# Performance work log

Measured on AMD Instinct MI355X. Metric: run time of the kernel, lower is better.

Reference implementation:

```python
import jax, jax.numpy as jnp
import numpy as np

DIM = 1024
DIM_INNER = 2048
B, S = 4, 4096


def setup_inputs() -> dict:
    key = jax.random.key(0)
    k1, k2, k3 = jax.random.split(key, 3)
    x = jax.random.normal(k1, (B, S, DIM), dtype=jnp.float32)
    # torch Linear weight init ~ U(-1/sqrt(fan_in), 1/sqrt(fan_in)); scaled normals are fine
    W_hg = jax.random.normal(k2, (DIM, 2 * DIM_INNER), dtype=jnp.float32) / np.sqrt(DIM)
    W_out = jax.random.normal(k3, (DIM_INNER, DIM), dtype=jnp.float32) / np.sqrt(DIM_INNER)
    return {"x": x, "W_hg": W_hg, "W_out": W_out}


def heinsen_associative_scan_log(log_coeffs, log_values):
    # a_star[t] = sum_{i<=t} log_coeffs[i]
    a_star = jnp.cumsum(log_coeffs, axis=1)
    log_h0_plus_b_star = jax.lax.cumlogsumexp(log_values - a_star, axis=1)
    return jnp.exp(a_star + log_h0_plus_b_star)


def reference(x, W_hg, W_out):
    # fused projection then split into hidden / gate, each [B, S, DIM_INNER]
    hg = jnp.einsum('bsd,de->bse', x, W_hg)
    hidden, gate = jnp.split(hg, 2, axis=-1)
    # seq_len > 1, prev_hidden = None path of the torch module
    log_z = jax.nn.log_sigmoid(gate)                 # log sigmoid(gate)
    log_coeffs = -jax.nn.softplus(gate)              # log(1 - sigmoid(gate))
    hidden_log = jnp.log(jax.nn.relu(hidden) + 0.5)  # log(g(hidden)) as coded (relu+0.5)
    log_values = hidden_log + log_z
    h = heinsen_associative_scan_log(log_coeffs, log_values)  # [B, S, DIM_INNER]
    out = jnp.einsum('bse,ed->bsd', h, W_out)
    return out
```

## Files before the change

kernel.cpp:

```cpp
#include <hip/hip_runtime.h>
#include <stdint.h>

#define DIMX 1024
#define DIM_INNER 2048
#define BATCH 4
#define SEQ 4096
#define M_TOTAL (BATCH * SEQ)
#define N_HG (2 * DIM_INNER)
#define NCHUNK 32
#define CLEN 128

typedef unsigned short u16;
typedef __attribute__((ext_vector_type(8))) short short8;
typedef __attribute__((ext_vector_type(4))) float floatx4;

__device__ __forceinline__ float bflo(uint32_t u) { return __uint_as_float(u << 16); }
__device__ __forceinline__ float bfhi(uint32_t u) { return __uint_as_float(u & 0xffff0000u); }
__device__ __forceinline__ uint32_t f2bf_bits(float f) {
    uint32_t u = __float_as_uint(f);
    return (u + 0x7fffu + ((u >> 16) & 1u)) >> 16;
}

__global__ __launch_bounds__(256) void prep(const float* __restrict__ x,
                                            const float* __restrict__ Whg,
                                            const float* __restrict__ Wout,
                                            u16* __restrict__ xb,
                                            u16* __restrict__ whgt,
                                            u16* __restrict__ woutt) {
    __shared__ float tile[64][65];
    const int bid = blockIdx.x;
    const int tid = threadIdx.x;
    if (bid < 2048) {
        const int n4 = M_TOTAL * DIMX / 4;
        const float4* in4 = (const float4*)x;
        ushort4* out4 = (ushort4*)xb;
        for (int i = bid * 256 + tid; i < n4; i += 2048 * 256) {
            float4 v = in4[i];
            ushort4 o;
            o.x = (u16)f2bf_bits(v.x);
            o.y = (u16)f2bf_bits(v.y);
            o.z = (u16)f2bf_bits(v.z);
            o.w = (u16)f2bf_bits(v.w);
            out4[i] = o;
        }
        return;
    }
    const float* in;
    u16* out;
    int R, C, tb;
    if (bid < 3072) {
        in = Whg; out = whgt; R = DIMX; C = N_HG; tb = bid - 2048;
    } else {
        in = Wout; out = woutt; R = DIM_INNER; C = DIMX; tb = bid - 3072;
    }
    const int tilesx = C / 64;
    const int c0 = (tb % tilesx) * 64, r0 = (tb / tilesx) * 64;
    const int tx = tid & 63, ty = tid >> 6;
#pragma unroll
    for (int i = ty; i < 64; i += 4)
        tile[i][tx] = in[(size_t)(r0 + i) * C + c0 + tx];
    __syncthreads();
#pragma unroll
    for (int i = ty; i < 64; i += 4)
        out[(size_t)(c0 + i) * R + r0 + tx] = (u16)f2bf_bits(tile[tx][i]);
}

__global__ __launch_bounds__(256, 2) void gemm1_k(const u16* __restrict__ A,
                                                  const u16* __restrict__ Bt,
                                                  uint32_t* __restrict__ av,
                                                  float2* __restrict__ sumAV) {
    __shared__ alignas(16) char smem[65536];
    u16* As = (u16*)smem;
    u16* Bh = (u16*)(smem + 8192);
    u16* Bg = (u16*)(smem + 16384);
    uint32_t* avl = (uint32_t*)smem;

    const int tid = threadIdx.x;
    const int lane = tid & 63;
    const int wave = tid >> 6;
    const int wm = (wave >> 1) * 64;
    const int wn = (wave & 1) * 64;
    const size_t m0 = (size_t)blockIdx.y * 128;
    const int n0 = blockIdx.x * 128;

    floatx4 acch[4][4], accg[4][4];
#pragma unroll
    for (int i = 0; i < 4; ++i)
#pragma unroll
        for (int j = 0; j < 4; ++j) {
            acch[i][j] = (floatx4){0.f, 0.f, 0.f, 0.f};
            accg[i][j] = (floatx4){0.f, 0.f, 0.f, 0.f};
        }

    const int srow = lane >> 2;
    const int scol = ((lane & 3) ^ ((srow >> 1) & 3)) * 8;
    const u16* Ag = A + m0 * DIMX + (size_t)(wave * 16 + srow) * DIMX + scol;
    const u16* Bhg = Bt + (size_t)n0 * DIMX + (size_t)(wave * 16 + srow) * DIMX + scol;
    const u16* Bgg = Bt + (size_t)(DIM_INNER + n0) * DIMX + (size_t)(wave * 16 + srow) * DIMX + scol;
    u16* Asw = As + (wave * 16) * 32;
    u16* Bhw = Bh + (wave * 16) * 32;
    u16* Bgw = Bg + (wave * 16) * 32;

    const int fr = lane & 15;
    const int kblk = lane >> 4;
    const int koff = (kblk ^ ((fr >> 1) & 3)) * 8;

    for (int k0 = 0; k0 < DIMX; k0 += 32) {
        __syncthreads();
#pragma unroll
        for (int i = 0; i < 2; ++i) {
            __builtin_amdgcn_global_load_lds(
                (const __attribute__((address_space(1))) uint32_t*)(const void*)(Ag + (size_t)i * 64 * DIMX + k0),
                (__attribute__((address_space(3))) uint32_t*)(void*)(Asw + i * 64 * 32), 16, 0, 0);
            __builtin_amdgcn_global_load_lds(
                (const __attribute__((address_space(1))) uint32_t*)(const void*)(Bhg + (size_t)i * 64 * DIMX + k0),
                (__attribute__((address_space(3))) uint32_t*)(void*)(Bhw + i * 64 * 32), 16, 0, 0);
            __builtin_amdgcn_global_load_lds(
                (const __attribute__((address_space(1))) uint32_t*)(const void*)(Bgg + (size_t)i * 64 * DIMX + k0),
                (__attribute__((address_space(3))) uint32_t*)(void*)(Bgw + i * 64 * 32), 16, 0, 0);
        }
        __syncthreads();

        short8 af[4], bhf[4], bgf[4];
#pragma unroll
        for (int i = 0; i < 4; ++i)
            af[i] = *(const short8*)(As + (wm + i * 16 + fr) * 32 + koff);
#pragma unroll
        for (int j = 0; j < 4; ++j) {
            bhf[j] = *(const short8*)(Bh + (wn + j * 16 + fr) * 32 + koff);
            bgf[j] = *(const short8*)(Bg + (wn + j * 16 + fr) * 32 + koff);
        }
#pragma unroll
        for (int i = 0; i < 4; ++i)
#pragma unroll
            for (int j = 0; j < 4; ++j) {
                acch[i][j] = __builtin_amdgcn_mfma_f32_16x16x32_bf16(af[i], bhf[j], acch[i][j], 0, 0, 0);
                accg[i][j] = __builtin_amdgcn_mfma_f32_16x16x32_bf16(af[i], bgf[j], accg[i][j], 0, 0, 0);
            }
    }
    __syncthreads();

    const int r0row = (lane >> 4) * 4;
#pragma unroll
    for (int i = 0; i < 4; ++i) {
#pragma unroll
        for (int r = 0; r < 4; ++r) {
            const int row = wm + i * 16 + r0row + r;
#pragma unroll
            for (int j = 0; j < 4; ++j) {
                const int col = wn + j * 16 + fr;
                float h = acch[i][j][r];
                float g = accg[i][j][r];
                g = fminf(fmaxf(g, -30.f), 30.f);
                float e = __expf(-g);
                float z = 1.f / (1.f + e);
                float a = e * z;
                float v = z * (fmaxf(h, 0.f) + 0.5f);
                uint32_t pk = f2bf_bits(a) | (f2bf_bits(v) << 16);
                avl[row * 128 + col] = pk;
                av[(m0 + row) * 2048 + n0 + col] = pk;
            }
        }
    }
    __syncthreads();

    const int col = tid & 127;
    const int rlo = (tid >> 7) * 64;
    float Aa = 1.f, Vv = 0.f;
#pragma unroll 8
    for (int j = 0; j < 64; ++j) {
        uint32_t pk = avl[(rlo + j) * 128 + col];
        float a = bflo(pk), v = bfhi(pk);
        Vv = fmaf(a, Vv, v);
        Aa *= a;
    }
    __syncthreads();
    if (tid < 128) {
        avl[col] = __float_as_uint(Aa);
        avl[128 + col] = __float_as_uint(Vv);
    }
    __syncthreads();
    if (tid >= 128) {
        float Al = __uint_as_float(avl[col]);
        float Vl = __uint_as_float(avl[128 + col]);
        float At = Al * Aa;
        float Vt = fmaf(Aa, Vl, Vv);
        const int chunk = (int)(m0 >> 7);
        sumAV[(size_t)chunk * 2048 + n0 + col] = (float2){At, Vt};
    }
}

__global__ __launch_bounds__(256, 2) void gemm2_k(const u16* __restrict__ A,
                                                  const u16* __restrict__ Bt,
                                                  float* __restrict__ C) {
    const int N = DIMX, K = DIM_INNER;
    __shared__ alignas(16) u16 As[256 * 32];
    __shared__ alignas(16) u16 Bs[128 * 32];

    const int tid = threadIdx.x;
    const int lane = tid & 63;
    const int wave = tid >> 6;
    const int wm = wave * 64;
    const size_t m0 = (size_t)blockIdx.y * 256;
    const size_t n0 = (size_t)blockIdx.x * 128;

    floatx4 acc[4][8];
#pragma unroll
    for (int i = 0; i < 4; ++i)
#pragma unroll
        for (int j = 0; j < 8; ++j) acc[i][j] = (floatx4){0.f, 0.f, 0.f, 0.f};

    const int srow = lane >> 2;
    const int scol = ((lane & 3) ^ ((srow >> 1) & 3)) * 8;
    const u16* Ag = A + (m0 + wave * 16 + srow) * K + scol;
    const u16* Bg = Bt + (n0 + wave * 16 + srow) * K + scol;
    u16* Asw = As + (wave * 16) * 32;
    u16* Bsw = Bs + (wave * 16) * 32;

    const int fr = lane & 15;
    const int kblk = lane >> 4;
    const int koff = (kblk ^ ((fr >> 1) & 3)) * 8;

    for (int k0 = 0; k0 < K; k0 += 32) {
        __syncthreads();
#pragma unroll
        for (int i = 0; i < 4; ++i)
            __builtin_amdgcn_global_load_lds(
                (const __attribute__((address_space(1))) uint32_t*)(const void*)(Ag + (size_t)i * 64 * K + k0),
                (__attribute__((address_space(3))) uint32_t*)(void*)(Asw + i * 64 * 32), 16, 0, 0);
#pragma unroll
        for (int i = 0; i < 2; ++i)
            __builtin_amdgcn_global_load_lds(
                (const __attribute__((address_space(1))) uint32_t*)(const void*)(Bg + (size_t)i * 64 * K + k0),
                (__attribute__((address_space(3))) uint32_t*)(void*)(Bsw + i * 64 * 32), 16, 0, 0);
        __syncthreads();

        short8 af[4], bf[8];
#pragma unroll
        for (int i = 0; i < 4; ++i)
            af[i] = *(const short8*)(As + (wm + i * 16 + fr) * 32 + koff);
#pragma unroll
        for (int j = 0; j < 8; ++j)
            bf[j] = *(const short8*)(Bs + (j * 16 + fr) * 32 + koff);
#pragma unroll
        for (int i = 0; i < 4; ++i)
#pragma unroll
            for (int j = 0; j < 8; ++j)
                acc[i][j] = __builtin_amdgcn_mfma_f32_16x16x32_bf16(af[i], bf[j], acc[i][j], 0, 0, 0);
    }

    const int r0row = (lane >> 4) * 4;
#pragma unroll
    for (int i = 0; i < 4; ++i)
#pragma unroll
        for (int r = 0; r < 4; ++r) {
            size_t row = m0 + wm + i * 16 + r0row + r;
#pragma unroll
            for (int j = 0; j < 8; ++j) {
                size_t col = n0 + j * 16 + fr;
                C[row * N + col] = acc[i][j][r];
            }
        }
}

__global__ __launch_bounds__(64) void scan_carry(const float2* __restrict__ sumAV,
                                                 float* __restrict__ carry) {
    const int g = blockIdx.x * 64 + threadIdx.x;
    const int b = g >> 11, c = g & 2047;
    float h = 0.f;
#pragma unroll 8
    for (int ch = 0; ch < NCHUNK; ++ch) {
        float2 s = sumAV[(size_t)(b * NCHUNK + ch) * 2048 + c];
        carry[(size_t)(b * NCHUNK + ch) * 2048 + c] = h;
        h = fmaf(s.x, h, s.y);
    }
}

__global__ __launch_bounds__(256) void scan_apply(const uint32_t* __restrict__ av,
                                                  const float* __restrict__ carry,
                                                  uint32_t* __restrict__ hbuf) {
    const int b = blockIdx.z, ch = blockIdx.y;
    const int c2 = blockIdx.x * 256 + threadIdx.x;
    const size_t rowbase = (size_t)b * SEQ + (size_t)ch * CLEN;
    const uint32_t* p = av + rowbase * 2048 + c2 * 2;
    uint32_t* q = hbuf + rowbase * 1024 + c2;
    const float2 cin = ((const float2*)carry)[(size_t)(b * NCHUNK + ch) * 1024 + c2];
    float h0 = cin.x, h1 = cin.y;

    uint2 buf[4];
#pragma unroll
    for (int t = 0; t < 4; ++t) buf[t] = *(const uint2*)(p + (size_t)t * 2048);

    for (int j0 = 0; j0 < CLEN; j0 += 4) {
        uint2 nxt[4];
        if (j0 + 4 < CLEN) {
#pragma unroll
            for (int t = 0; t < 4; ++t)
                nxt[t] = *(const uint2*)(p + (size_t)(j0 + 4 + t) * 2048);
        }
#pragma unroll
        for (int t = 0; t < 4; ++t) {
            float a0 = bflo(buf[t].x), v0 = bfhi(buf[t].x);
            float a1 = bflo(buf[t].y), v1 = bfhi(buf[t].y);
            h0 = fmaf(a0, h0, v0);
            h1 = fmaf(a1, h1, v1);
            q[(size_t)(j0 + t) * 1024] = f2bf_bits(h0) | (f2bf_bits(h1) << 16);
        }
#pragma unroll
        for (int t = 0; t < 4; ++t) buf[t] = nxt[t];
    }
}

extern "C" void kernel_launch(void* const* d_in, const int* in_sizes, int n_in,
                              void* d_out, int out_size, void* d_ws, size_t ws_size,
                              hipStream_t stream) {
    const float* x = (const float*)d_in[0];
    const float* Whg = (const float*)d_in[1];
    const float* Wout = (const float*)d_in[2];

    char* ws = (char*)d_ws;
    size_t off = 0;
    u16* xb = (u16*)(ws + off);        off += (size_t)M_TOTAL * DIMX * 2;
    u16* whgt = (u16*)(ws + off);      off += (size_t)N_HG * DIMX * 2;
    u16* woutt = (u16*)(ws + off);     off += (size_t)DIMX * DIM_INNER * 2;
    uint32_t* av = (uint32_t*)(ws + off); off += (size_t)M_TOTAL * DIM_INNER * 4;
    uint32_t* hbuf = (uint32_t*)(ws + off); off += (size_t)M_TOTAL * DIM_INNER * 2;
    float2* sumAV = (float2*)(ws + off); off += (size_t)BATCH * NCHUNK * DIM_INNER * 8;
    float* carry = (float*)whgt;

    prep<<<2048 + 1024 + 512, 256, 0, stream>>>(x, Whg, Wout, xb, whgt, woutt);

    gemm1_k<<<dim3(16, 128), 256, 0, stream>>>(xb, whgt, av, sumAV);

    scan_carry<<<128, 64, 0, stream>>>(sumAV, carry);
    scan_apply<<<dim3(4, NCHUNK, BATCH), 256, 0, stream>>>(av, carry, hbuf);

    gemm2_k<<<dim3(DIMX / 128, M_TOTAL / 256), 256, 0, stream>>>((const u16*)hbuf, woutt, (float*)d_out);
}
```

Measured before the change: 418.8 us.

## Pipeline both GEMMs with 4-stage async LDS buffering and larger 512-thread tiles

Both GEMM kernels move to 512-thread blocks with larger output tiles (256x128 for gemm1, 256x256 for gemm2). Global-to-LDS loads now run through a 4-deep ring of buffers with vmcnt-based waits, so the next tiles load while MFMAs run. MFMA sections are wrapped in s_setprio raises. Gemm1's epilogue now produces two chunk summaries per block. The aim is to hide load latency and raise reuse per LDS byte, at the cost of more registers, a full 128KB of LDS per block, and fewer blocks in the grid.

```diff
diff --git a/kernel.cpp b/kernel.cpp
--- a/kernel.cpp
+++ b/kernel.cpp
@@ -20,6 +20,14 @@
     uint32_t u = __float_as_uint(f);
     return (u + 0x7fffu + ((u >> 16) & 1u)) >> 16;
 }
+
+#define GCAST(p) (const __attribute__((address_space(1))) uint32_t*)(const void*)(p)
+#define LCAST(p) (__attribute__((address_space(3))) uint32_t*)(void*)(p)
+#define SYNCG(N)                                                              \
+    do {                                                                      \
+        asm volatile("s_waitcnt vmcnt(" #N ") lgkmcnt(0)" ::: "memory");      \
+        __builtin_amdgcn_s_barrier();                                         \
+    } while (0)
 
 __global__ __launch_bounds__(256) void prep(const float* __restrict__ x,
                                             const float* __restrict__ Whg,
@@ -65,90 +73,98 @@
         out[(size_t)(c0 + i) * R + r0 + tx] = (u16)f2bf_bits(tile[tx][i]);
 }
 
-__global__ __launch_bounds__(256, 2) void gemm1_k(const u16* __restrict__ A,
+__global__ __launch_bounds__(512, 2) void gemm1_k(const u16* __restrict__ A,
                                                   const u16* __restrict__ Bt,
                                                   uint32_t* __restrict__ av,
                                                   float2* __restrict__ sumAV) {
-    __shared__ alignas(16) char smem[65536];
-    u16* As = (u16*)smem;
-    u16* Bh = (u16*)(smem + 8192);
-    u16* Bg = (u16*)(smem + 16384);
-    uint32_t* avl = (uint32_t*)smem;
-
+    __shared__ alignas(16) u16 smem[65536];
     const int tid = threadIdx.x;
     const int lane = tid & 63;
     const int wave = tid >> 6;
-    const int wm = (wave >> 1) * 64;
-    const int wn = (wave & 1) * 64;
-    const size_t m0 = (size_t)blockIdx.y * 128;
+    const int wr = wave >> 2;
+    const int wc = wave & 3;
+    const size_t m0 = (size_t)blockIdx.y * 256;
     const int n0 = blockIdx.x * 128;
 
-    floatx4 acch[4][4], accg[4][4];
-#pragma unroll
-    for (int i = 0; i < 4; ++i)
-#pragma unroll
-        for (int j = 0; j < 4; ++j) {
+    floatx4 acch[8][2], accg[8][2];
+#pragma unroll
+    for (int i = 0; i < 8; ++i)
+#pragma unroll
+        for (int j = 0; j < 2; ++j) {
             acch[i][j] = (floatx4){0.f, 0.f, 0.f, 0.f};
             accg[i][j] = (floatx4){0.f, 0.f, 0.f, 0.f};
         }
 
     const int srow = lane >> 2;
-    const int scol = ((lane & 3) ^ ((srow >> 1) & 3)) * 8;
-    const u16* Ag = A + m0 * DIMX + (size_t)(wave * 16 + srow) * DIMX + scol;
-    const u16* Bhg = Bt + (size_t)n0 * DIMX + (size_t)(wave * 16 + srow) * DIMX + scol;
-    const u16* Bgg = Bt + (size_t)(DIM_INNER + n0) * DIMX + (size_t)(wave * 16 + srow) * DIMX + scol;
-    u16* Asw = As + (wave * 16) * 32;
-    u16* Bhw = Bh + (wave * 16) * 32;
-    u16* Bgw = Bg + (wave * 16) * 32;
+    const int ssw = ((lane & 3) ^ ((srow >> 1) & 3)) * 8;
+    const u16* Ag = A + (m0 + wave * 16 + srow) * DIMX + ssw;
+    const u16* Bhg = Bt + ((size_t)(n0 + wave * 16 + srow)) * DIMX + ssw;
+    const u16* Bgg = Bt + ((size_t)(DIM_INNER + n0 + wave * 16 + srow)) * DIMX + ssw;
 
     const int fr = lane & 15;
-    const int kblk = lane >> 4;
-    const int koff = (kblk ^ ((fr >> 1) & 3)) * 8;
-
-    for (int k0 = 0; k0 < DIMX; k0 += 32) {
-        __syncthreads();
-#pragma unroll
-        for (int i = 0; i < 2; ++i) {
-            __builtin_amdgcn_global_load_lds(
-                (const __attribute__((address_space(1))) uint32_t*)(const void*)(Ag + (size_t)i * 64 * DIMX + k0),
-                (__attribute__((address_space(3))) uint32_t*)(void*)(Asw + i * 64 * 32), 16, 0, 0);
-            __builtin_amdgcn_global_load_lds(
-                (const __attribute__((address_space(1))) uint32_t*)(const void*)(Bhg + (size_t)i * 64 * DIMX + k0),
-                (__attribute__((address_space(3))) uint32_t*)(void*)(Bhw + i * 64 * 32), 16, 0, 0);
-            __builtin_amdgcn_global_load_lds(
-                (const __attribute__((address_space(1))) uint32_t*)(const void*)(Bgg + (size_t)i * 64 * DIMX + k0),
-                (__attribute__((address_space(3))) uint32_t*)(void*)(Bgw + i * 64 * 32), 16, 0, 0);
-        }
-        __syncthreads();
-
-        short8 af[4], bhf[4], bgf[4];
-#pragma unroll
-        for (int i = 0; i < 4; ++i)
-            af[i] = *(const short8*)(As + (wm + i * 16 + fr) * 32 + koff);
-#pragma unroll
-        for (int j = 0; j < 4; ++j) {
-            bhf[j] = *(const short8*)(Bh + (wn + j * 16 + fr) * 32 + koff);
-            bgf[j] = *(const short8*)(Bg + (wn + j * 16 + fr) * 32 + koff);
-        }
-#pragma unroll
-        for (int i = 0; i < 4; ++i)
-#pragma unroll
-            for (int j = 0; j < 4; ++j) {
-                acch[i][j] = __builtin_amdgcn_mfma_f32_16x16x32_bf16(af[i], bhf[j], acch[i][j], 0, 0, 0);
-                accg[i][j] = __builtin_amdgcn_mfma_f32_16x16x32_bf16(af[i], bgf[j], accg[i][j], 0, 0, 0);
-            }
-    }
-    __syncthreads();
-
+    const int koff = ((lane >> 4) ^ ((fr >> 1) & 3)) * 8;
+
+#define STAGE1(u)                                                                          \
+    do {                                                                                   \
+        const int q_ = (u) & 3;                                                            \
+        const int k0_ = (u) * 32;                                                          \
+        u16* b_ = smem + q_ * 16384;                                                       \
+        __builtin_amdgcn_global_load_lds(GCAST(Ag + k0_), LCAST(b_ + wave * 512), 16, 0, 0);                \
+        __builtin_amdgcn_global_load_lds(GCAST(Ag + (size_t)128 * DIMX + k0_),             \
+                                         LCAST(b_ + 4096 + wave * 512), 16, 0, 0);         \
+        __builtin_amdgcn_global_load_lds(GCAST(Bhg + k0_), LCAST(b_ + 8192 + wave * 512), 16, 0, 0);        \
+        __builtin_amdgcn_global_load_lds(GCAST(Bgg + k0_), LCAST(b_ + 12288 + wave * 512), 16, 0, 0);       \
+    } while (0)
+
+#define TILE1(u, DOSTAGE)                                                                  \
+    do {                                                                                   \
+        const u16* As_ = smem + ((u) & 3) * 16384;                                         \
+        const u16* Bh_ = As_ + 8192;                                                       \
+        const u16* Bg_ = As_ + 12288;                                                      \
+        short8 af_[8], bh_[2], bg_[2];                                                     \
+        _Pragma("unroll") for (int j_ = 0; j_ < 2; ++j_) {                                 \
+            bh_[j_] = *(const short8*)(Bh_ + (wc * 32 + j_ * 16 + fr) * 32 + koff);        \
+            bg_[j_] = *(const short8*)(Bg_ + (wc * 32 + j_ * 16 + fr) * 32 + koff);        \
+        }                                                                                  \
+        _Pragma("unroll") for (int i_ = 0; i_ < 8; ++i_)                                   \
+            af_[i_] = *(const short8*)(As_ + (wr * 128 + i_ * 16 + fr) * 32 + koff);       \
+        if (DOSTAGE) STAGE1((u) + 3);                                                      \
+        __builtin_amdgcn_s_setprio(1);                                                     \
+        _Pragma("unroll") for (int i_ = 0; i_ < 8; ++i_)                                   \
+            _Pragma("unroll") for (int j_ = 0; j_ < 2; ++j_) {                             \
+                acch[i_][j_] =                                                             \
+                    __builtin_amdgcn_mfma_f32_16x16x32_bf16(af_[i_], bh_[j_], acch[i_][j_], 0, 0, 0); \
+                accg[i_][j_] =                                                             \
+                    __builtin_amdgcn_mfma_f32_16x16x32_bf16(af_[i_], bg_[j_], accg[i_][j_], 0, 0, 0); \
+            }                                                                              \
+        __builtin_amdgcn_s_setprio(0);                                                     \
+    } while (0)
+
+    STAGE1(0);
+    STAGE1(1);
+    STAGE1(2);
+    for (int t = 0; t < 29; ++t) {
+        SYNCG(8);
+        TILE1(t, 1);
+    }
+    SYNCG(8);
+    TILE1(29, 0);
+    SYNCG(4);
+    TILE1(30, 0);
+    SYNCG(0);
+    TILE1(31, 0);
+    __syncthreads();
+
+    uint32_t* avl = (uint32_t*)smem;
     const int r0row = (lane >> 4) * 4;
 #pragma unroll
-    for (int i = 0; i < 4; ++i) {
+    for (int i = 0; i < 8; ++i) {
 #pragma unroll
         for (int r = 0; r < 4; ++r) {
-            const int row = wm + i * 16 + r0row + r;
-#pragma unroll
-            for (int j = 0; j < 4; ++j) {
-                const int col = wn + j * 16 + fr;
+            const int row = wr * 128 + i * 16 + r0row + r;
+#pragma unroll
+            for (int j = 0; j < 2; ++j) {
+                const int col = wc * 32 + j * 16 + fr;
                 float h = acch[i][j][r];
                 float g = accg[i][j][r];
                 g = fminf(fmaxf(g, -30.f), 30.f);
@@ -164,103 +180,122 @@
     }
     __syncthreads();
 
-    const int col = tid & 127;
-    const int rlo = (tid >> 7) * 64;
+    const int chl = tid >> 8;
+    const int t2 = tid & 255;
+    const int col = t2 & 127;
+    const int rlo = (t2 >> 7) * 64;
     float Aa = 1.f, Vv = 0.f;
 #pragma unroll 8
     for (int j = 0; j < 64; ++j) {
-        uint32_t pk = avl[(rlo + j) * 128 + col];
+        uint32_t pk = avl[(chl * 128 + rlo + j) * 128 + col];
         float a = bflo(pk), v = bfhi(pk);
         Vv = fmaf(a, Vv, v);
         Aa *= a;
     }
     __syncthreads();
-    if (tid < 128) {
-        avl[col] = __float_as_uint(Aa);
-        avl[128 + col] = __float_as_uint(Vv);
-    }
-    __syncthreads();
-    if (tid >= 128) {
-        float Al = __uint_as_float(avl[col]);
-        float Vl = __uint_as_float(avl[128 + col]);
+    if (rlo == 0) {
+        avl[chl * 256 + col] = __float_as_uint(Aa);
+        avl[chl * 256 + 128 + col] = __float_as_uint(Vv);
+    }
+    __syncthreads();
+    if (rlo != 0) {
+        float Al = __uint_as_float(avl[chl * 256 + col]);
+        float Vl = __uint_as_float(avl[chl * 256 + 128 + col]);
         float At = Al * Aa;
         float Vt = fmaf(Aa, Vl, Vv);
-        const int chunk = (int)(m0 >> 7);
+        const int chunk = (int)(m0 >> 7) + chl;
         sumAV[(size_t)chunk * 2048 + n0 + col] = (float2){At, Vt};
     }
-}
-
-__global__ __launch_bounds__(256, 2) void gemm2_k(const u16* __restrict__ A,
+#undef STAGE1
+#undef TILE1
+}
+
+__global__ __launch_bounds__(512, 2) void gemm2_k(const u16* __restrict__ A,
                                                   const u16* __restrict__ Bt,
                                                   float* __restrict__ C) {
     const int N = DIMX, K = DIM_INNER;
-    __shared__ alignas(16) u16 As[256 * 32];
-    __shared__ alignas(16) u16 Bs[128 * 32];
-
+    __shared__ alignas(16) u16 smem[65536];
     const int tid = threadIdx.x;
     const int lane = tid & 63;
     const int wave = tid >> 6;
-    const int wm = wave * 64;
+    const int wr = wave >> 2;
+    const int wc = wave & 3;
     const size_t m0 = (size_t)blockIdx.y * 256;
-    const size_t n0 = (size_t)blockIdx.x * 128;
-
-    floatx4 acc[4][8];
-#pragma unroll
-    for (int i = 0; i < 4; ++i)
-#pragma unroll
-        for (int j = 0; j < 8; ++j) acc[i][j] = (floatx4){0.f, 0.f, 0.f, 0.f};
+    const size_t n0 = (size_t)blockIdx.x * 256;
+
+    floatx4 acc[8][4];
+#pragma unroll
+    for (int i = 0; i < 8; ++i)
+#pragma unroll
+        for (int j = 0; j < 4; ++j) acc[i][j] = (floatx4){0.f, 0.f, 0.f, 0.f};
 
     const int srow = lane >> 2;
-    const int scol = ((lane & 3) ^ ((srow >> 1) & 3)) * 8;
-    const u16* Ag = A + (m0 + wave * 16 + srow) * K + scol;
-    const u16* Bg = Bt + (n0 + wave * 16 + srow) * K + scol;
-    u16* Asw = As + (wave * 16) * 32;
-    u16* Bsw = Bs + (wave * 16) * 32;
+    const int ssw = ((lane & 3) ^ ((srow >> 1) & 3)) * 8;
+    const u16* Ag = A + (m0 + wave * 16 + srow) * K + ssw;
+    const u16* Bg2 = Bt + (n0 + wave * 16 + srow) * K + ssw;
 
     const int fr = lane & 15;
-    const int kblk = lane >> 4;
-    const int koff = (kblk ^ ((fr >> 1) & 3)) * 8;
-
-    for (int k0 = 0; k0 < K; k0 += 32) {
-        __syncthreads();
-#pragma unroll
-        for (int i = 0; i < 4; ++i)
-            __builtin_amdgcn_global_load_lds(
-                (const __attribute__((address_space(1))) uint32_t*)(const void*)(Ag + (size_t)i * 64 * K + k0),
-                (__attribute__((address_space(3))) uint32_t*)(void*)(Asw + i * 64 * 32), 16, 0, 0);
-#pragma unroll
-        for (int i = 0; i < 2; ++i)
-            __builtin_amdgcn_global_load_lds(
-                (const __attribute__((address_space(1))) uint32_t*)(const void*)(Bg + (size_t)i * 64 * K + k0),
-                (__attribute__((address_space(3))) uint32_t*)(void*)(Bsw + i * 64 * 32), 16, 0, 0);
-        __syncthreads();
-
-        short8 af[4], bf[8];
-#pragma unroll
-        for (int i = 0; i < 4; ++i)
-            af[i] = *(const short8*)(As + (wm + i * 16 + fr) * 32 + koff);
-#pragma unroll
-        for (int j = 0; j < 8; ++j)
-            bf[j] = *(const short8*)(Bs + (j * 16 + fr) * 32 + koff);
-#pragma unroll
-        for (int i = 0; i < 4; ++i)
-#pragma unroll
-            for (int j = 0; j < 8; ++j)
-                acc[i][j] = __builtin_amdgcn_mfma_f32_16x16x32_bf16(af[i], bf[j], acc[i][j], 0, 0, 0);
-    }
+    const int koff = ((lane >> 4) ^ ((fr >> 1) & 3)) * 8;
+
+#define STAGE2(u)                                                                          \
+    do {                                                                                   \
+        const int q_ = (u) & 3;                                                            \
+        const int k0_ = (u) * 32;                                                          \
+        u16* b_ = smem + q_ * 16384;                                                       \
+        __builtin_amdgcn_global_load_lds(GCAST(Ag + k0_), LCAST(b_ + wave * 512), 16, 0, 0);            \
+        __builtin_amdgcn_global_load_lds(GCAST(Ag + (size_t)128 * K + k0_),                \
+                                         LCAST(b_ + 4096 + wave * 512), 16, 0, 0);         \
+        __builtin_amdgcn_global_load_lds(GCAST(Bg2 + k0_), LCAST(b_ + 8192 + wave * 512), 16, 0, 0);    \
+        __builtin_amdgcn_global_load_lds(GCAST(Bg2 + (size_t)128 * K + k0_),               \
+                                         LCAST(b_ + 12288 + wave * 512), 16, 0, 0);        \
+    } while (0)
+
+#define TILE2(u, DOSTAGE)                                                                  \
+    do {                                                                                   \
+        const u16* As_ = smem + ((u) & 3) * 16384;                                         \
+        const u16* Bs_ = As_ + 8192;                                                       \
+        short8 af_[8], bf_[4];                                                             \
+        _Pragma("unroll") for (int j_ = 0; j_ < 4; ++j_)                                   \
+            bf_[j_] = *(const short8*)(Bs_ + (wc * 64 + j_ * 16 + fr) * 32 + koff);        \
+        _Pragma("unroll") for (int i_ = 0; i_ < 8; ++i_)                                   \
+            af_[i_] = *(const short8*)(As_ + (wr * 128 + i_ * 16 + fr) * 32 + koff);       \
+        if (DOSTAGE) STAGE2((u) + 3);                                                      \
+        __builtin_amdgcn_s_setprio(1);                                                     \
+        _Pragma("unroll") for (int i_ = 0; i_ < 8; ++i_)                                   \
+            _Pragma("unroll") for (int j_ = 0; j_ < 4; ++j_)                               \
+                acc[i_][j_] =                                                              \
+                    __builtin_amdgcn_mfma_f32_16x16x32_bf16(af_[i_], bf_[j_], acc[i_][j_], 0, 0, 0); \
+        __builtin_amdgcn_s_setprio(0);                                                     \
+    } while (0)
+
+    STAGE2(0);
+    STAGE2(1);
+    STAGE2(2);
+    for (int t = 0; t < 61; ++t) {
+        SYNCG(8);
+        TILE2(t, 1);
+    }
+    SYNCG(8);
+    TILE2(61, 0);
+    SYNCG(4);
+    TILE2(62, 0);
+    SYNCG(0);
+    TILE2(63, 0);
 
     const int r0row = (lane >> 4) * 4;
 #pragma unroll
-    for (int i = 0; i < 4; ++i)
+    for (int i = 0; i < 8; ++i)
 #pragma unroll
         for (int r = 0; r < 4; ++r) {
-            size_t row = m0 + wm + i * 16 + r0row + r;
-#pragma unroll
-            for (int j = 0; j < 8; ++j) {
-                size_t col = n0 + j * 16 + fr;
+            size_t row = m0 + wr * 128 + i * 16 + r0row + r;
+#pragma unroll
+            for (int j = 0; j < 4; ++j) {
+                size_t col = n0 + wc * 64 + j * 16 + fr;
                 C[row * N + col] = acc[i][j][r];
             }
         }
+#undef STAGE2
+#undef TILE2
 }
 
 __global__ __launch_bounds__(64) void scan_carry(const float2* __restrict__ sumAV,
@@ -330,10 +365,10 @@
 
     prep<<<2048 + 1024 + 512, 256, 0, stream>>>(x, Whg, Wout, xb, whgt, woutt);
 
-    gemm1_k<<<dim3(16, 128), 256, 0, stream>>>(xb, whgt, av, sumAV);
+    gemm1_k<<<dim3(16, 64), 512, 0, stream>>>(xb, whgt, av, sumAV);
 
     scan_carry<<<128, 64, 0, stream>>>(sumAV, carry);
     scan_apply<<<dim3(4, NCHUNK, BATCH), 256, 0, stream>>>(av, carry, hbuf);
 
-    gemm2_k<<<dim3(DIMX / 128, M_TOTAL / 256), 256, 0, stream>>>((const u16*)hbuf, woutt, (float*)d_out);
-}
+    gemm2_k<<<dim3(DIMX / 256, M_TOTAL / 256), 512, 0, stream>>>((const u16*)hbuf, woutt, (float*)d_out);
+}
```

Result: faster. 393.4 us (-6.1%).
